# Performance work log

Measured on AMD Instinct MI355X. Metric: run time of the kernel, lower is better.

The kernel has to match this reference:

```python
import jax, jax.numpy as jnp
import numpy as np

IN_SIZE = 1024
HIDDEN = 50
OUT_DIM = 8
BATCH = 16384
BN_EPS = 1e-5


def _gf(h, W1, b1, W2, b2):
    # graph_fusion: Linear -> LeakyReLU(0.2) -> Linear -> Tanh
    t = h @ W1 + b1
    t = jnp.where(t > 0, t, 0.2 * t)
    return jnp.tanh(t @ W2 + b2)


def _lrelu(z):
    return jnp.where(z > 0, z, 0.01 * z)  # F.leaky_relu default slope


def _dot(p, q):
    return jnp.sum(p * q, axis=-1)  # batched [B,1,D]@[B,D,1] -> [B]


def setup_inputs() -> dict:
    key = jax.random.key(0)
    ks = jax.random.split(key, 16)
    d, h, o = IN_SIZE, HIDDEN, OUT_DIM
    s = lambda n: 1.0 / np.sqrt(n)
    return {
        "x": jax.random.normal(ks[0], (BATCH, 3, d), jnp.float32),
        "att_W": jax.random.normal(ks[1], (d, 1), jnp.float32) * s(d),
        "att_b": jnp.zeros((1,), jnp.float32),
        "gf_W1": jax.random.normal(ks[2], (2 * d, 64), jnp.float32) * s(2 * d),
        "gf_b1": jnp.zeros((64,), jnp.float32),
        "gf_W2": jax.random.normal(ks[3], (64, d), jnp.float32) * s(64),
        "gf_b2": jnp.zeros((d,), jnp.float32),
        "bn_gamma": jnp.ones((3 * d,), jnp.float32),
        "bn_beta": jnp.zeros((3 * d,), jnp.float32),
        "l1_W": jax.random.normal(ks[4], (3 * d, h), jnp.float32) * s(3 * d),
        "l1_b": jnp.zeros((h,), jnp.float32),
        "l2_W": jax.random.normal(ks[5], (h, h), jnp.float32) * s(h),
        "l2_b": jnp.zeros((h,), jnp.float32),
        "l3_W": jax.random.normal(ks[6], (h, o), jnp.float32) * s(h),
        "l3_b": jnp.zeros((o,), jnp.float32),
    }


def _forward(x, att_W, att_b, gf_W1, gf_b1, gf_W2, gf_b2,
             bn_gamma, bn_beta, l1_W, l1_b, l2_W, l2_b, l3_W, l3_b):
    a1, v1, l1_ = x[:, 0, :], x[:, 1, :], x[:, 2, :]
    gf = lambda p, q: _gf(jnp.concatenate([p, q], axis=1), gf_W1, gf_b1, gf_W2, gf_b2)

    # unimodal attention weights, softmax over the 3 modalities
    att = jnp.tanh(x @ att_W + att_b)[..., 0]          # [B,3]
    w_uni = jax.nn.softmax(att, axis=1)                # [B,3]
    sa, sv, sl = w_uni[:, 0], w_uni[:, 1], w_uni[:, 2]
    unimodal = (sa[:, None] * a1 + sv[:, None] * v1 + sl[:, None] * l1_) / 3.0

    a = jax.nn.softmax(a1, axis=1)
    v = jax.nn.softmax(v1, axis=1)
    l = jax.nn.softmax(l1_, axis=1)
    sav = (sa + sv) / (_dot(a, v) + 0.5)
    sal = (sa + sl) / (_dot(a, l) + 0.5)
    svl = (sl + sv) / (_dot(v, l) + 0.5)
    w_bi = jax.nn.softmax(jnp.stack([sav, sal, svl], axis=1), axis=1)  # [B,3]

    a_v = _lrelu(w_bi[:, 0:1] * gf(a1, v1))
    a_l = _lrelu(w_bi[:, 1:2] * gf(a1, l1_))
    v_l = _lrelu(w_bi[:, 2:3] * gf(v1, l1_))
    bimodal = (a_v + a_l + v_l) / 3.0

    a_v2 = jax.nn.softmax(a_v, axis=1)
    a_l2 = jax.nn.softmax(a_l, axis=1)
    v_l2 = jax.nn.softmax(v_l, axis=1)
    savvl = (sav + svl) / (_dot(a_v2, v_l2) + 0.5)
    saavl = (sav + sal) / (_dot(a_v2, a_l2) + 0.5)
    savll = (sal + svl) / (_dot(a_l2, v_l2) + 0.5)
    savl = (sav + sl) / (_dot(a_v2, l) + 0.5)
    salv = (sal + sv) / (_dot(a_l2, v) + 0.5)
    svla = (sa + svl) / (_dot(v_l2, a) + 0.5)
    w_tri = jax.nn.softmax(
        jnp.stack([savvl, saavl, savll, savl, salv, svla], axis=1), axis=1)  # [B,6]

    avvl = _lrelu(w_tri[:, 0:1] * gf(a_v, v_l))
    aavl = _lrelu(w_tri[:, 1:2] * gf(a_v, a_l))
    avll = _lrelu(w_tri[:, 2:3] * gf(v_l, a_l))
    avl = _lrelu(w_tri[:, 3:4] * gf(a_v, l1_))
    alv = _lrelu(w_tri[:, 4:5] * gf(a_l, v1))
    vla = _lrelu(w_tri[:, 5:6] * gf(v_l, a1))
    trimodal = (avvl + aavl + avll + avl + alv + vla) / 6.0

    fusion = jnp.concatenate([unimodal, bimodal, trimodal], axis=1)  # [B,3*in]
    # BatchNorm1d in eval mode: running_mean=0, running_var=1
    fusion = fusion * (bn_gamma / jnp.sqrt(1.0 + BN_EPS)) + bn_beta
    y = jnp.tanh(fusion @ l1_W + l1_b)
    y = jnp.tanh(y @ l2_W + l2_b)
    y2 = jax.nn.softmax(y @ l3_W + l3_b, axis=1)
    total_weights = jnp.concatenate([w_uni, w_bi, w_tri], axis=1)  # [B,12]
    return y2, total_weights


def reference(x, att_W, att_b, gf_W1, gf_b1, gf_W2, gf_b2,
              bn_gamma, bn_beta, l1_W, l1_b, l2_W, l2_b, l3_W, l3_b):
    return _forward(x, att_W, att_b, gf_W1, gf_b1, gf_W2, gf_b2,
                    bn_gamma, bn_beta, l1_W, l1_b, l2_W, l2_b, l3_W, l3_b)
```

## Files before the change

kernel.cpp:

```cpp
#include <hip/hip_runtime.h>
#include <math.h>

#define NB 16384
#define DD 1024
#define KF 5120

typedef unsigned short u16;
typedef unsigned int u32;
typedef __attribute__((ext_vector_type(8))) short bf16x8;
typedef __attribute__((ext_vector_type(4))) float f32x4;

__device__ __forceinline__ float bf2f(u16 u){
  return __uint_as_float(((unsigned)u) << 16);
}
__device__ __forceinline__ u16 f2bf(float f){
  unsigned u = __float_as_uint(f);
  return (u16)((u + 0x7fffu + ((u >> 16) & 1u)) >> 16);
}
__device__ __forceinline__ u16 f2bf_tr(float f){
  return (u16)(__float_as_uint(f) >> 16);
}
__device__ __forceinline__ u32 pack2bf(float a, float b){
  return (u32)f2bf(a) | ((u32)f2bf(b) << 16);
}
__device__ __forceinline__ float fast_tanh(float x){
  float e = __expf(2.0f * x);
  return 1.0f - 2.0f * __builtin_amdgcn_rcpf(e + 1.0f);
}
__device__ __forceinline__ float wredsum(float x){
  #pragma unroll
  for(int o = 32; o >= 1; o >>= 1) x += __shfl_xor(x, o);
  return x;
}
__device__ __forceinline__ float wredmax(float x){
  #pragma unroll
  for(int o = 32; o >= 1; o >>= 1) x = fmaxf(x, __shfl_xor(x, o));
  return x;
}
__device__ __forceinline__ void gll16(const void* g, void* l){
  __builtin_amdgcn_global_load_lds(
      (const __attribute__((address_space(1))) u32*)g,
      (__attribute__((address_space(3))) u32*)l, 16, 0, 0);
}

__global__ __launch_bounds__(256) void k1_stats(
    const float* __restrict__ x, const float* __restrict__ attW,
    const float* __restrict__ attb, float* __restrict__ stats,
    u16* __restrict__ Fcat, u16* __restrict__ xb, float* __restrict__ tw)
{
  int wave = threadIdx.x >> 6, lane = threadIdx.x & 63;
  int r = blockIdx.x * 4 + wave;
  const float2* xr  = (const float2*)(x + (size_t)r * 3 * DD);
  const float2* aw2 = (const float2*)attW;
  float2 a[8], v[8], l[8];
  float dA=0.f,dV=0.f,dL=0.f, mA=-1e30f,mV=-1e30f,mL=-1e30f;
  #pragma unroll
  for(int i = 0; i < 8; i++){
    int k2 = lane + i*64;
    a[i] = xr[k2]; v[i] = xr[512+k2]; l[i] = xr[1024+k2];
    float2 w = aw2[k2];
    dA = fmaf(a[i].x, w.x, fmaf(a[i].y, w.y, dA));
    dV = fmaf(v[i].x, w.x, fmaf(v[i].y, w.y, dV));
    dL = fmaf(l[i].x, w.x, fmaf(l[i].y, w.y, dL));
    mA = fmaxf(mA, fmaxf(a[i].x, a[i].y));
    mV = fmaxf(mV, fmaxf(v[i].x, v[i].y));
    mL = fmaxf(mL, fmaxf(l[i].x, l[i].y));
  }
  dA = wredsum(dA); dV = wredsum(dV); dL = wredsum(dL);
  mA = wredmax(mA); mV = wredmax(mV); mL = wredmax(mL);

  u32* xbw = (u32*)(xb + (size_t)3*r*DD);
  #pragma unroll
  for(int i = 0; i < 8; i++){
    int k2 = lane + i*64;
    xbw[k2]      = pack2bf(a[i].x, a[i].y);
    xbw[512+k2]  = pack2bf(v[i].x, v[i].y);
    xbw[1024+k2] = pack2bf(l[i].x, l[i].y);
  }

  float Sa=0.f,Sv=0.f,Sl=0.f,Eav=0.f,Eal=0.f,Evl=0.f;
  #pragma unroll
  for(int i = 0; i < 8; i++){
    float eax = __expf(a[i].x-mA), eay = __expf(a[i].y-mA);
    float evx = __expf(v[i].x-mV), evy = __expf(v[i].y-mV);
    float elx = __expf(l[i].x-mL), ely = __expf(l[i].y-mL);
    Sa += eax+eay; Sv += evx+evy; Sl += elx+ely;
    Eav += eax*evx + eay*evy; Eal += eax*elx + eay*ely; Evl += evx*elx + evy*ely;
  }
  Sa = wredsum(Sa); Sv = wredsum(Sv); Sl = wredsum(Sl);
  Eav = wredsum(Eav); Eal = wredsum(Eal); Evl = wredsum(Evl);

  float ab = attb[0];
  float ta = fast_tanh(dA + ab), tv = fast_tanh(dV + ab), tl = fast_tanh(dL + ab);
  float mm = fmaxf(ta, fmaxf(tv, tl));
  float e0 = __expf(ta-mm), e1 = __expf(tv-mm), e2 = __expf(tl-mm);
  float ss = e0 + e1 + e2;
  float sa = e0/ss, sv = e1/ss, sl = e2/ss;
  float dav = Eav/(Sa*Sv), dal = Eal/(Sa*Sl), dvl = Evl/(Sv*Sl);
  float sav = (sa+sv)/(dav+0.5f);
  float sal = (sa+sl)/(dal+0.5f);
  float svl = (sv+sl)/(dvl+0.5f);
  float m2 = fmaxf(sav, fmaxf(sal, svl));
  float f0 = __expf(sav-m2), f1 = __expf(sal-m2), f2 = __expf(svl-m2);
  float s2 = f0 + f1 + f2;
  float wb0 = f0/s2, wb1 = f1/s2, wb2 = f2/s2;

  if(lane == 0){
    float* st = stats + (size_t)r*24;
    st[0]=sa; st[1]=sv; st[2]=sl;
    st[3]=wb0; st[4]=wb1; st[5]=wb2;
    st[6]=sav; st[7]=sal; st[8]=svl;
    st[9]=mA; st[10]=Sa; st[11]=mV; st[12]=Sv; st[13]=mL; st[14]=Sl;
    float* twr = tw + (size_t)r*12;
    twr[0]=sa; twr[1]=sv; twr[2]=sl; twr[3]=wb0; twr[4]=wb1; twr[5]=wb2;
  }
  u32* uniw = (u32*)(Fcat + (size_t)r*KF);
  #pragma unroll
  for(int i = 0; i < 8; i++){
    int k2 = lane + i*64;
    float ux = (sa*a[i].x + sv*v[i].x + sl*l[i].x) * (1.0f/3.0f);
    float uy = (sa*a[i].y + sv*v[i].y + sl*l[i].y) * (1.0f/3.0f);
    uniw[k2] = pack2bf(ux, uy);
  }
}

__global__ __launch_bounds__(256) void kprew_b1(
    const float* __restrict__ W1, u16* __restrict__ Wb1)
{
  int idx = blockIdx.x * 256 + threadIdx.x;
  int n = idx >> 10, k = idx & 1023;
  float v = (n < 64) ? W1[(size_t)k*64 + n] : W1[(size_t)(1024+k)*64 + (n-64)];
  Wb1[idx] = f2bf(v);
}

__global__ __launch_bounds__(256) void kprew_w2t(
    const float* __restrict__ W2, u16* __restrict__ W2T)
{
  int idx = blockIdx.x * 256 + threadIdx.x;
  int c = idx >> 6, k = idx & 63;
  W2T[idx] = f2bf(W2[(size_t)k*DD + c]);
}

template<int FCAT>
__global__ __launch_bounds__(256) void kg1v3(
    const u16* __restrict__ src, const u16* __restrict__ Wb1,
    float* __restrict__ UV)
{
  __shared__ u16 Asm[2][64*64];
  int tid = threadIdx.x;
  int wv = tid >> 6, lane = tid & 63;
  int fr = lane & 15, kg = lane >> 4;
  int mb = blockIdx.x * 64;

  int r8 = lane >> 3, p = lane & 7;
  int sp = p ^ r8;
  int m0 = mb + (2*wv)*8 + r8;
  int m1 = mb + (2*wv+1)*8 + r8;
  size_t b0, b1;
  if(FCAT){
    int R0 = m0/3, R1 = m1/3;
    b0 = (size_t)R0*KF + (size_t)(1 + (m0 - 3*R0))*1024;
    b1 = (size_t)R1*KF + (size_t)(1 + (m1 - 3*R1))*1024;
  } else {
    b0 = (size_t)m0*1024;
    b1 = (size_t)m1*1024;
  }
  const u16* gsrc0 = src + b0 + sp*8;
  const u16* gsrc1 = src + b1 + sp*8;

  f32x4 acc[4][2];
  #pragma unroll
  for(int rf = 0; rf < 4; rf++)
    #pragma unroll
    for(int nf = 0; nf < 2; nf++) acc[rf][nf] = (f32x4){0.f,0.f,0.f,0.f};

  gll16(gsrc0, &Asm[0][(2*wv)*512]);
  gll16(gsrc1, &Asm[0][(2*wv+1)*512]);
  __syncthreads();

  int buf = 0;
  for(int ci = 0; ci < 16; ci++){
    int k0 = ci*64;
    if(ci < 15){
      gll16(gsrc0 + k0 + 64, &Asm[buf^1][(2*wv)*512]);
      gll16(gsrc1 + k0 + 64, &Asm[buf^1][(2*wv+1)*512]);
    }
    #pragma unroll
    for(int ks = 0; ks < 2; ks++){
      bf16x8 a[4];
      #pragma unroll
      for(int rf = 0; rf < 4; rf++){
        int row = rf*16 + fr;
        int slot = (ks*4 + kg) ^ (row & 7);
        a[rf] = *(const bf16x8*)&Asm[buf][row*64 + slot*8];
      }
      #pragma unroll
      for(int nf = 0; nf < 2; nf++){
        int col = wv*32 + nf*16 + fr;
        bf16x8 b = *(const bf16x8*)&Wb1[(size_t)col*1024 + k0 + ks*32 + kg*8];
        #pragma unroll
        for(int rf = 0; rf < 4; rf++)
          acc[rf][nf] = __builtin_amdgcn_mfma_f32_16x16x32_bf16(a[rf], b, acc[rf][nf], 0, 0, 0);
      }
    }
    __syncthreads();
    buf ^= 1;
  }

  #pragma unroll
  for(int rf = 0; rf < 4; rf++)
    #pragma unroll
    for(int nf = 0; nf < 2; nf++)
      #pragma unroll
      for(int q = 0; q < 4; q++)
        UV[(size_t)(mb + rf*16 + kg*4 + q)*128 + wv*32 + nf*16 + fr] = acc[rf][nf][q];
}

template<int P, int SUM>
__global__ __launch_bounds__(256) void kL2v4(
    const float* __restrict__ UVA, const float* __restrict__ UVB,
    const u16* __restrict__ W2T, const float* __restrict__ b1,
    const float* __restrict__ b2, const float* __restrict__ stats,
    u16* __restrict__ Fcat)
{
  const int NP = SUM ? 1 : P;
  __shared__ u16 Tsm[P][16][64];
  __shared__ u16 Osm[NP][16][264];
  __shared__ float stw[16][8];
  int tid = threadIdx.x;
  int wv = tid >> 6, lane = tid & 63;
  int fr = lane & 15, kg = lane >> 4;
  int Rb = blockIdx.x * 16;
  int cb = blockIdx.y * 256 + wv * 64;

  const int NG = P*16*8;
  for(int i = tid; i < NG; i += 256){
    int g = i & 7, r = (i >> 3) & 15, p = i >> 7;
    int R = Rb + r;
    int up, vp; const float* VBb;
    if(P == 3){
      up = (p == 2) ? 1 : 0;
      vp = (p == 0) ? 1 : 2;
      VBb = UVA;
    } else {
      up = (0x210200 >> (p*4)) & 15;
      vp = (0x012112 >> (p*4)) & 15;
      VBb = (p < 3) ? UVA : UVB;
    }
    const float* Up = UVA + (size_t)(3*R + up)*128 + g*8;
    const float* Vp = VBb + (size_t)(3*R + vp)*128 + 64 + g*8;
    float4 u0 = *(const float4*)Up, u1 = *(const float4*)(Up+4);
    float4 v0 = *(const float4*)Vp, v1 = *(const float4*)(Vp+4);
    float4 bb0 = *(const float4*)(b1 + g*8), bb1 = *(const float4*)(b1 + g*8 + 4);
    float t[8] = {u0.x+v0.x+bb0.x, u0.y+v0.y+bb0.y, u0.z+v0.z+bb0.z, u0.w+v0.w+bb0.w,
                  u1.x+v1.x+bb1.x, u1.y+v1.y+bb1.y, u1.z+v1.z+bb1.z, u1.w+v1.w+bb1.w};
    bf16x8 o;
    #pragma unroll
    for(int j = 0; j < 8; j++){
      float tv = t[j] > 0.f ? t[j] : 0.2f*t[j];
      o[j] = (short)f2bf_tr(tv);
    }
    *(bf16x8*)&Tsm[p][r][(g ^ (r & 7))*8] = o;
  }
  if(tid < 16*P){
    int r = tid / P, p = tid - r*P;
    stw[r][p] = stats[(size_t)(Rb + r)*24 + (SUM ? 15 : 3) + p];
  }
  __syncthreads();

  f32x4 acc[P][4];
  #pragma unroll
  for(int p = 0; p < P; p++)
    #pragma unroll
    for(int cf = 0; cf < 4; cf++) acc[p][cf] = (f32x4){0.f,0.f,0.f,0.f};

  #pragma unroll
  for(int ks = 0; ks < 2; ks++){
    bf16x8 a[P];
    #pragma unroll
    for(int p = 0; p < P; p++)
      a[p] = *(const bf16x8*)&Tsm[p][fr][(((ks<<2)+kg) ^ (fr & 7))*8];
    #pragma unroll
    for(int cf = 0; cf < 4; cf++){
      bf16x8 b = *(const bf16x8*)&W2T[(size_t)(cb + cf*16 + fr)*64 + ks*32 + kg*8];
      #pragma unroll
      for(int p = 0; p < P; p++)
        acc[p][cf] = __builtin_amdgcn_mfma_f32_16x16x32_bf16(a[p], b, acc[p][cf], 0, 0, 0);
    }
  }

  #pragma unroll
  for(int q = 0; q < 4; q++){
    int row = kg*4 + q;
    #pragma unroll
    for(int cf = 0; cf < 4; cf++){
      int cloc = wv*64 + cf*16 + fr;
      float b2c = b2[blockIdx.y*256 + cloc];
      if(SUM){
        float s = 0.f;
        #pragma unroll
        for(int p = 0; p < P; p++){
          float g = stw[row][p] * fast_tanh(acc[p][cf][q] + b2c);
          s += g > 0.f ? g : 0.01f*g;
        }
        Osm[0][row][cloc] = f2bf(s * (1.0f/6.0f));
      } else {
        #pragma unroll
        for(int p = 0; p < P; p++){
          float g = stw[row][p] * fast_tanh(acc[p][cf][q] + b2c);
          float val = g > 0.f ? g : 0.01f*g;
          Osm[p][row][cloc] = f2bf(val);
        }
      }
    }
  }
  __syncthreads();
  {
    int orow = tid >> 4, oc16 = (tid & 15) * 16;
    #pragma unroll
    for(int p = 0; p < NP; p++){
      bf16x8 o0 = *(const bf16x8*)&Osm[p][orow][oc16];
      bf16x8 o1 = *(const bf16x8*)&Osm[p][orow][oc16 + 8];
      size_t off = (size_t)(Rb + orow)*KF + (SUM ? 4096 : (size_t)(1+p)*1024)
                 + blockIdx.y*256 + oc16;
      *(bf16x8*)&Fcat[off]     = o0;
      *(bf16x8*)&Fcat[off + 8] = o1;
    }
  }
}

__global__ __launch_bounds__(256) void k3s_stats2(
    const u16* __restrict__ Fcat, const u16* __restrict__ xb,
    float* __restrict__ stats, float* __restrict__ tw)
{
  int wave = threadIdx.x >> 6, lane = threadIdx.x & 63;
  int r = blockIdx.x * 4 + wave;
  const u32* pv = (const u32*)(Fcat + (size_t)r*KF + 1024);
  const u32* xv = (const u32*)(xb + (size_t)3*r*DD);
  float2 av[8], al[8], vl[8];
  float mav=-1e30f, mal=-1e30f, mvl=-1e30f;
  #pragma unroll
  for(int i = 0; i < 8; i++){
    int k2 = lane + i*64;
    u32 wa = pv[k2], wb = pv[512+k2], wc = pv[1024+k2];
    av[i] = make_float2(bf2f((u16)wa), bf2f((u16)(wa>>16)));
    al[i] = make_float2(bf2f((u16)wb), bf2f((u16)(wb>>16)));
    vl[i] = make_float2(bf2f((u16)wc), bf2f((u16)(wc>>16)));
    mav = fmaxf(mav, fmaxf(av[i].x, av[i].y));
    mal = fmaxf(mal, fmaxf(al[i].x, al[i].y));
    mvl = fmaxf(mvl, fmaxf(vl[i].x, vl[i].y));
  }
  mav = wredmax(mav); mal = wredmax(mal); mvl = wredmax(mvl);

  float* st = stats + (size_t)r*24;
  float sa=st[0], sv=st[1], sl=st[2];
  float sav=st[6], sal=st[7], svl=st[8];
  float mA=st[9], Sa=st[10], mV=st[11], Sv=st[12], mL=st[13], Sl=st[14];

  float Savv=0.f,Sall=0.f,Svll=0.f,E1=0.f,E2=0.f,E3=0.f,E4=0.f,E5=0.f,E6=0.f;
  #pragma unroll
  for(int i = 0; i < 8; i++){
    int k2 = lane + i*64;
    u32 xa = xv[k2], xvv = xv[512+k2], xl = xv[1024+k2];
    float a1x = bf2f((u16)xa),  a1y = bf2f((u16)(xa>>16));
    float v1x = bf2f((u16)xvv), v1y = bf2f((u16)(xvv>>16));
    float l1x = bf2f((u16)xl),  l1y = bf2f((u16)(xl>>16));
    float eavx = __expf(av[i].x-mav), eavy = __expf(av[i].y-mav);
    float ealx = __expf(al[i].x-mal), ealy = __expf(al[i].y-mal);
    float evlx = __expf(vl[i].x-mvl), evly = __expf(vl[i].y-mvl);
    Savv += eavx+eavy; Sall += ealx+ealy; Svll += evlx+evly;
    float eax = __expf(a1x-mA), eay = __expf(a1y-mA);
    float evx = __expf(v1x-mV), evy = __expf(v1y-mV);
    float elx = __expf(l1x-mL), ely = __expf(l1y-mL);
    E1 += eavx*evlx + eavy*evly; E2 += eavx*ealx + eavy*ealy; E3 += ealx*evlx + ealy*evly;
    E4 += eavx*elx + eavy*ely;   E5 += ealx*evx + ealy*evy;   E6 += evlx*eax + evly*eay;
  }
  Savv = wredsum(Savv); Sall = wredsum(Sall); Svll = wredsum(Svll);
  E1 = wredsum(E1); E2 = wredsum(E2); E3 = wredsum(E3);
  E4 = wredsum(E4); E5 = wredsum(E5); E6 = wredsum(E6);

  float d1 = E1/(Savv*Svll), d2 = E2/(Savv*Sall), d3 = E3/(Sall*Svll);
  float d4 = E4/(Savv*Sl),   d5 = E5/(Sall*Sv),   d6 = E6/(Svll*Sa);
  float t0 = (sav+svl)/(d1+0.5f);
  float t1 = (sav+sal)/(d2+0.5f);
  float t2 = (sal+svl)/(d3+0.5f);
  float t3 = (sav+sl)/(d4+0.5f);
  float t4 = (sal+sv)/(d5+0.5f);
  float t5 = (sa+svl)/(d6+0.5f);
  float mx = fmaxf(fmaxf(fmaxf(t0,t1),fmaxf(t2,t3)),fmaxf(t4,t5));
  float g0=__expf(t0-mx),g1=__expf(t1-mx),g2=__expf(t2-mx);
  float g3=__expf(t3-mx),g4=__expf(t4-mx),g5=__expf(t5-mx);
  float gs = g0+g1+g2+g3+g4+g5;
  if(lane == 0){
    float wt[6] = {g0/gs,g1/gs,g2/gs,g3/gs,g4/gs,g5/gs};
    float* twr = tw + (size_t)r*12;
    #pragma unroll
    for(int p = 0; p < 6; p++){ st[15+p] = wt[p]; twr[6+p] = wt[p]; }
  }
}

__global__ __launch_bounds__(256) void k6_prew(
    const float* __restrict__ gamma, const float* __restrict__ l1W,
    u16* __restrict__ WpT)
{
  int kk = blockIdx.x * 256 + threadIdx.x;
  int j  = blockIdx.y;
  const float gsc = 1.0f / sqrtf(1.0f + 1e-5f);
  int korig; float sc;
  if(kk < 1024){ korig = kk; sc = 1.f; }
  else if(kk < 4096){ korig = 1024 + ((kk - 1024) & 1023); sc = 1.0f/3.0f; }
  else { korig = 2048 + (kk - 4096); sc = 1.f; }
  float v = (j < 50) ? l1W[(size_t)korig*50 + j] * gamma[korig] * gsc * sc : 0.f;
  WpT[(size_t)j*KF + kk] = f2bf(v);
}

__global__ __launch_bounds__(256) void k6_preb(
    const float* __restrict__ beta, const float* __restrict__ l1W,
    const float* __restrict__ l1b, float* __restrict__ bp)
{
  __shared__ float red[4][64];
  int j = threadIdx.x & 63, seg = threadIdx.x >> 6;
  float s = 0.f;
  if(j < 50){
    for(int k = seg*768; k < seg*768 + 768; k++)
      s = fmaf(beta[k], l1W[(size_t)k*50 + j], s);
  }
  red[seg][j] = s;
  __syncthreads();
  if(seg == 0){
    float t = red[0][j] + red[1][j] + red[2][j] + red[3][j];
    bp[j] = (j < 50) ? (l1b[j] + t) : 0.f;
  }
}

__global__ __launch_bounds__(256) void k6v4(
    const u16* __restrict__ Fcat, const u16* __restrict__ WpT,
    const float* __restrict__ bp,
    const float* __restrict__ l2W, const float* __restrict__ l2b,
    const float* __restrict__ l3W, const float* __restrict__ l3b,
    float* __restrict__ y2out)
{
  __shared__ __align__(16) char smem[37952];
  u16*  Asm = (u16*)smem;
  float* W2s = (float*)(smem + 16384);
  float* W3s = (float*)(smem + 16384 + 12800);
  float* Ys  = (float*)smem;
  float* Ys2 = (float*)(smem + 16384 + 12800 + 1600);

  int tid = threadIdx.x;
  int wv = tid >> 6, lane = tid & 63;
  int fr = lane & 15, kg = lane >> 4;
  int rb = blockIdx.x * 32;

  for(int t = tid; t < 3200; t += 256){
    int c = t & 63;
    W2s[t] = (c < 50) ? l2W[(t >> 6)*50 + c] : 0.f;
  }
  for(int t = tid; t < 400; t += 256) W3s[t] = l3W[t];

  int r8 = lane >> 3, pp = lane & 7;
  int sp = pp ^ r8;
  const u16* gsrc = Fcat + (size_t)(rb + wv*8 + r8)*KF + sp*8;
  const u16* bptr = WpT  + (size_t)(wv*16 + fr)*KF + kg*8;

  f32x4 acc[2];
  acc[0] = (f32x4){0.f,0.f,0.f,0.f};
  acc[1] = (f32x4){0.f,0.f,0.f,0.f};

  gll16(gsrc,      &Asm[wv*1024]);
  gll16(gsrc + 64, &Asm[wv*1024 + 512]);
  __syncthreads();

  int buf = 0;
  for(int ci = 0; ci < 40; ci++){
    int k0 = ci*128;
    if(ci < 39){
      gll16(gsrc + k0 + 128, &Asm[(buf^1)*4096 + wv*1024]);
      gll16(gsrc + k0 + 192, &Asm[(buf^1)*4096 + wv*1024 + 512]);
    }
    #pragma unroll
    for(int kh = 0; kh < 2; kh++){
      #pragma unroll
      for(int ks = 0; ks < 2; ks++){
        bf16x8 b = *(const bf16x8*)(bptr + k0 + kh*64 + ks*32);
        #pragma unroll
        for(int rf = 0; rf < 2; rf++){
          int row = rf*16 + fr;
          int slot = ((ks<<2) + kg) ^ (row & 7);
          bf16x8 a = *(const bf16x8*)&Asm[buf*4096 + (row>>3)*1024 + kh*512
                                          + (row & 7)*64 + slot*8];
          acc[rf] = __builtin_amdgcn_mfma_f32_16x16x32_bf16(a, b, acc[rf], 0, 0, 0);
        }
      }
    }
    __syncthreads();
    buf ^= 1;
  }

  {
    int col = wv*16 + fr;
    float bpc = bp[col];
    #pragma unroll
    for(int rf = 0; rf < 2; rf++)
      #pragma unroll
      for(int q = 0; q < 4; q++){
        int row = rf*16 + kg*4 + q;
        if(col < 50) Ys[row*56 + col] = fast_tanh(acc[rf][q] + bpc);
      }
  }
  __syncthreads();

  {
    int r = tid >> 3, cg = (tid & 7) * 7;
    float a2[7] = {0,0,0,0,0,0,0};
    for(int k = 0; k < 50; k++){
      float yv = Ys[r*56 + k];
      #pragma unroll
      for(int c = 0; c < 7; c++) a2[c] = fmaf(yv, W2s[k*64 + cg + c], a2[c]);
    }
    #pragma unroll
    for(int c = 0; c < 7; c++){
      int cc = cg + c;
      if(cc < 50) Ys2[r*56 + cc] = fast_tanh(a2[c] + l2b[cc]);
    }
  }
  __syncthreads();

  {
    int r = tid >> 3, c = tid & 7;
    float z = l3b[c];
    for(int k = 0; k < 50; k++) z = fmaf(Ys2[r*56 + k], W3s[k*8 + c], z);
    float m = z;
    m = fmaxf(m, __shfl_xor(m, 1));
    m = fmaxf(m, __shfl_xor(m, 2));
    m = fmaxf(m, __shfl_xor(m, 4));
    float e = __expf(z - m);
    float s = e;
    s += __shfl_xor(s, 1); s += __shfl_xor(s, 2); s += __shfl_xor(s, 4);
    y2out[(size_t)(rb + r)*8 + c] = e / s;
  }
}

extern "C" void kernel_launch(void* const* d_in, const int* in_sizes, int n_in,
                              void* d_out, int out_size, void* d_ws, size_t ws_size,
                              hipStream_t stream)
{
  (void)in_sizes; (void)n_in; (void)out_size; (void)ws_size;
  const float* x    = (const float*)d_in[0];
  const float* attW = (const float*)d_in[1];
  const float* attb = (const float*)d_in[2];
  const float* gfW1 = (const float*)d_in[3];
  const float* gfb1 = (const float*)d_in[4];
  const float* gfW2 = (const float*)d_in[5];
  const float* gfb2 = (const float*)d_in[6];
  const float* bng  = (const float*)d_in[7];
  const float* bnb  = (const float*)d_in[8];
  const float* l1W  = (const float*)d_in[9];
  const float* l1b  = (const float*)d_in[10];
  const float* l2W  = (const float*)d_in[11];
  const float* l2b  = (const float*)d_in[12];
  const float* l3W  = (const float*)d_in[13];
  const float* l3b  = (const float*)d_in[14];

  float* out = (float*)d_out;
  float* tw  = out + (size_t)NB*8;

  float* ws    = (float*)d_ws;
  float* stats = ws;
  float* UV1   = stats + (size_t)NB*24;
  float* UV2   = UV1 + (size_t)3*NB*128;
  float* bp    = UV2 + (size_t)3*NB*128;
  u16* WpT     = (u16*)(bp + 64);
  u16* Wb1     = WpT + (size_t)64*KF;
  u16* W2T     = Wb1 + (size_t)128*1024;
  u16* Fcat    = W2T + (size_t)1024*64;
  u16* xb      = Fcat + (size_t)NB*KF;

  k1_stats<<<dim3(NB/4), dim3(256), 0, stream>>>(x, attW, attb, stats, Fcat, xb, tw);
  kprew_b1<<<dim3(512), dim3(256), 0, stream>>>(gfW1, Wb1);
  kprew_w2t<<<dim3(256), dim3(256), 0, stream>>>(gfW2, W2T);
  k6_prew<<<dim3(20, 64), dim3(256), 0, stream>>>(bng, l1W, WpT);
  k6_preb<<<dim3(1), dim3(256), 0, stream>>>(bnb, l1W, l1b, bp);

  kg1v3<0><<<dim3(3*NB/64), dim3(256), 0, stream>>>(xb, Wb1, UV1);
  kL2v4<3,0><<<dim3(NB/16, 4), dim3(256), 0, stream>>>(UV1, UV1, W2T, gfb1, gfb2, stats, Fcat);
  k3s_stats2<<<dim3(NB/4), dim3(256), 0, stream>>>(Fcat, xb, stats, tw);
  kg1v3<1><<<dim3(3*NB/64), dim3(256), 0, stream>>>(Fcat, Wb1, UV2);
  kL2v4<6,1><<<dim3(NB/16, 4), dim3(256), 0, stream>>>(UV2, UV1, W2T, gfb1, gfb2, stats, Fcat);
  k6v4<<<dim3(NB/32), dim3(256), 0, stream>>>(Fcat, WpT, bp, l2W, l2b, l3W, l3b, out);
}
```

Baseline: 406.7 us.

## Fuse fusion-layer partial GEMM into gf epilogues with atomic accumulation

The bimodal and trimodal contributions to the first classifier layer are now computed inside the graph-fusion epilogue kernels. Each block multiplies its output tile by the matching slice of the folded weight and atomically adds the result into a per-row accumulator. The final kernel therefore only streams the unimodal 1024 columns instead of the full 5120-wide concatenation. The trimodal block is no longer written to the concat buffer, and the weight-prep kernels are merged into one launch. The stats2 kernel also drops its max-subtraction pass for the bimodal softmaxes, which relies on those values being bounded, and the change adds atomic traffic plus some bf16 truncation.

```diff
diff --git a/kernel.cpp b/kernel.cpp
--- a/kernel.cpp
+++ b/kernel.cpp
@@ -43,10 +43,57 @@
       (__attribute__((address_space(3))) u32*)l, 16, 0, 0);
 }
 
+__global__ __launch_bounds__(256) void kpre(
+    const float* __restrict__ W1, const float* __restrict__ W2,
+    const float* __restrict__ gamma, const float* __restrict__ beta,
+    const float* __restrict__ l1W, const float* __restrict__ l1b,
+    u16* __restrict__ Wb1, u16* __restrict__ W2T, u16* __restrict__ WpT,
+    float* __restrict__ bp, float* __restrict__ y1g)
+{
+  __shared__ float red[4][64];
+  int b = blockIdx.x, tid = threadIdx.x;
+  if(b < 512){
+    int idx = b*256 + tid;
+    int n = idx >> 10, k = idx & 1023;
+    float v = (n < 64) ? W1[(size_t)k*64 + n] : W1[(size_t)(1024+k)*64 + (n-64)];
+    Wb1[idx] = f2bf(v);
+  } else if(b < 768){
+    int idx = (b-512)*256 + tid;
+    int c = idx >> 6, k = idx & 63;
+    W2T[idx] = f2bf(W2[(size_t)k*DD + c]);
+  } else if(b < 768 + 1280){
+    int idx = (b-768)*256 + tid;
+    int j = idx / KF, kk = idx - j*KF;
+    const float gsc = 1.0f / sqrtf(1.0f + 1e-5f);
+    int korig; float sc;
+    if(kk < 1024){ korig = kk; sc = 1.f; }
+    else if(kk < 4096){ korig = 1024 + ((kk - 1024) & 1023); sc = 1.0f/3.0f; }
+    else { korig = 2048 + (kk - 4096); sc = 1.f; }
+    float v = (j < 50) ? l1W[(size_t)korig*50 + j] * gamma[korig] * gsc * sc : 0.f;
+    WpT[(size_t)j*KF + kk] = f2bf(v);
+  } else if(b < 768 + 1280 + 1024){
+    int idx = (b - 2048)*256 + tid;
+    ((float4*)y1g)[idx] = make_float4(0.f,0.f,0.f,0.f);
+  } else {
+    int j = tid & 63, seg = tid >> 6;
+    float s = 0.f;
+    if(j < 50){
+      for(int k = seg*768; k < seg*768 + 768; k++)
+        s = fmaf(beta[k], l1W[(size_t)k*50 + j], s);
+    }
+    red[seg][j] = s;
+    __syncthreads();
+    if(seg == 0){
+      float t = red[0][j] + red[1][j] + red[2][j] + red[3][j];
+      bp[j] = (j < 50) ? (l1b[j] + t) : 0.f;
+    }
+  }
+}
+
 __global__ __launch_bounds__(256) void k1_stats(
     const float* __restrict__ x, const float* __restrict__ attW,
     const float* __restrict__ attb, float* __restrict__ stats,
-    u16* __restrict__ Fcat, u16* __restrict__ xb, float* __restrict__ tw)
+    u16* __restrict__ uniB, u16* __restrict__ xb, float* __restrict__ tw)
 {
   int wave = threadIdx.x >> 6, lane = threadIdx.x & 63;
   int r = blockIdx.x * 4 + wave;
@@ -114,7 +161,7 @@
     float* twr = tw + (size_t)r*12;
     twr[0]=sa; twr[1]=sv; twr[2]=sl; twr[3]=wb0; twr[4]=wb1; twr[5]=wb2;
   }
-  u32* uniw = (u32*)(Fcat + (size_t)r*KF);
+  u32* uniw = (u32*)(uniB + (size_t)r*DD);
   #pragma unroll
   for(int i = 0; i < 8; i++){
     int k2 = lane + i*64;
@@ -122,23 +169,6 @@
     float uy = (sa*a[i].y + sv*v[i].y + sl*l[i].y) * (1.0f/3.0f);
     uniw[k2] = pack2bf(ux, uy);
   }
-}
-
-__global__ __launch_bounds__(256) void kprew_b1(
-    const float* __restrict__ W1, u16* __restrict__ Wb1)
-{
-  int idx = blockIdx.x * 256 + threadIdx.x;
-  int n = idx >> 10, k = idx & 1023;
-  float v = (n < 64) ? W1[(size_t)k*64 + n] : W1[(size_t)(1024+k)*64 + (n-64)];
-  Wb1[idx] = f2bf(v);
-}
-
-__global__ __launch_bounds__(256) void kprew_w2t(
-    const float* __restrict__ W2, u16* __restrict__ W2T)
-{
-  int idx = blockIdx.x * 256 + threadIdx.x;
-  int c = idx >> 6, k = idx & 63;
-  W2T[idx] = f2bf(W2[(size_t)k*DD + c]);
 }
 
 template<int FCAT>
@@ -217,21 +247,21 @@
 }
 
 template<int P, int SUM>
-__global__ __launch_bounds__(256) void kL2v4(
+__global__ __launch_bounds__(256) void kL2v5(
     const float* __restrict__ UVA, const float* __restrict__ UVB,
-    const u16* __restrict__ W2T, const float* __restrict__ b1,
-    const float* __restrict__ b2, const float* __restrict__ stats,
-    u16* __restrict__ Fcat)
-{
-  const int NP = SUM ? 1 : P;
+    const u16* __restrict__ W2T, const u16* __restrict__ WpT,
+    const float* __restrict__ b1, const float* __restrict__ b2,
+    const float* __restrict__ stats, u16* __restrict__ Fcat,
+    float* __restrict__ y1g)
+{
+  const int NO = SUM ? 1 : 4;
   __shared__ u16 Tsm[P][16][64];
-  __shared__ u16 Osm[NP][16][264];
+  __shared__ u16 Osm[NO][16][264];
   __shared__ float stw[16][8];
   int tid = threadIdx.x;
   int wv = tid >> 6, lane = tid & 63;
   int fr = lane & 15, kg = lane >> 4;
   int Rb = blockIdx.x * 16;
-  int cb = blockIdx.y * 256 + wv * 64;
 
   const int NG = P*16*8;
   for(int i = tid; i < NG; i += 256){
@@ -282,7 +312,8 @@
       a[p] = *(const bf16x8*)&Tsm[p][fr][(((ks<<2)+kg) ^ (fr & 7))*8];
     #pragma unroll
     for(int cf = 0; cf < 4; cf++){
-      bf16x8 b = *(const bf16x8*)&W2T[(size_t)(cb + cf*16 + fr)*64 + ks*32 + kg*8];
+      bf16x8 b = *(const bf16x8*)&W2T[(size_t)(blockIdx.y*256 + wv*64 + cf*16 + fr)*64
+                                      + ks*32 + kg*8];
       #pragma unroll
       for(int p = 0; p < P; p++)
         acc[p][cf] = __builtin_amdgcn_mfma_f32_16x16x32_bf16(a[p], b, acc[p][cf], 0, 0, 0);
@@ -303,33 +334,53 @@
           float g = stw[row][p] * fast_tanh(acc[p][cf][q] + b2c);
           s += g > 0.f ? g : 0.01f*g;
         }
-        Osm[0][row][cloc] = f2bf(s * (1.0f/6.0f));
+        Osm[0][row][cloc] = f2bf_tr(s * (1.0f/6.0f));
       } else {
+        float sm = 0.f;
         #pragma unroll
         for(int p = 0; p < P; p++){
           float g = stw[row][p] * fast_tanh(acc[p][cf][q] + b2c);
           float val = g > 0.f ? g : 0.01f*g;
           Osm[p][row][cloc] = f2bf(val);
+          sm += val;
         }
+        Osm[3][row][cloc] = f2bf_tr(sm);
       }
     }
   }
   __syncthreads();
-  {
+
+  if(!SUM){
     int orow = tid >> 4, oc16 = (tid & 15) * 16;
     #pragma unroll
-    for(int p = 0; p < NP; p++){
+    for(int p = 0; p < 3; p++){
       bf16x8 o0 = *(const bf16x8*)&Osm[p][orow][oc16];
       bf16x8 o1 = *(const bf16x8*)&Osm[p][orow][oc16 + 8];
-      size_t off = (size_t)(Rb + orow)*KF + (SUM ? 4096 : (size_t)(1+p)*1024)
-                 + blockIdx.y*256 + oc16;
+      size_t off = (size_t)(Rb + orow)*KF + (size_t)(1+p)*1024 + blockIdx.y*256 + oc16;
       *(bf16x8*)&Fcat[off]     = o0;
       *(bf16x8*)&Fcat[off + 8] = o1;
     }
   }
-}
-
-__global__ __launch_bounds__(256) void k3s_stats2(
+
+  {
+    size_t kbase = (SUM ? 4096 : 1024) + (size_t)blockIdx.y*256;
+    const u16* bptr = WpT + (size_t)(wv*16 + fr)*KF + kbase + kg*8;
+    f32x4 accy = (f32x4){0.f,0.f,0.f,0.f};
+    #pragma unroll
+    for(int kq = 0; kq < 4; kq++)
+      #pragma unroll
+      for(int ks = 0; ks < 2; ks++){
+        bf16x8 a = *(const bf16x8*)&Osm[NO-1][fr][kq*64 + ks*32 + kg*8];
+        bf16x8 b = *(const bf16x8*)(bptr + kq*64 + ks*32);
+        accy = __builtin_amdgcn_mfma_f32_16x16x32_bf16(a, b, accy, 0, 0, 0);
+      }
+    #pragma unroll
+    for(int q = 0; q < 4; q++)
+      atomicAdd(&y1g[(size_t)(Rb + kg*4 + q)*64 + wv*16 + fr], accy[q]);
+  }
+}
+
+__global__ __launch_bounds__(256) void k3s_v2(
     const u16* __restrict__ Fcat, const u16* __restrict__ xb,
     float* __restrict__ stats, float* __restrict__ tw)
 {
@@ -337,20 +388,6 @@
   int r = blockIdx.x * 4 + wave;
   const u32* pv = (const u32*)(Fcat + (size_t)r*KF + 1024);
   const u32* xv = (const u32*)(xb + (size_t)3*r*DD);
-  float2 av[8], al[8], vl[8];
-  float mav=-1e30f, mal=-1e30f, mvl=-1e30f;
-  #pragma unroll
-  for(int i = 0; i < 8; i++){
-    int k2 = lane + i*64;
-    u32 wa = pv[k2], wb = pv[512+k2], wc = pv[1024+k2];
-    av[i] = make_float2(bf2f((u16)wa), bf2f((u16)(wa>>16)));
-    al[i] = make_float2(bf2f((u16)wb), bf2f((u16)(wb>>16)));
-    vl[i] = make_float2(bf2f((u16)wc), bf2f((u16)(wc>>16)));
-    mav = fmaxf(mav, fmaxf(av[i].x, av[i].y));
-    mal = fmaxf(mal, fmaxf(al[i].x, al[i].y));
-    mvl = fmaxf(mvl, fmaxf(vl[i].x, vl[i].y));
-  }
-  mav = wredmax(mav); mal = wredmax(mal); mvl = wredmax(mvl);
 
   float* st = stats + (size_t)r*24;
   float sa=st[0], sv=st[1], sl=st[2];
@@ -361,17 +398,15 @@
   #pragma unroll
   for(int i = 0; i < 8; i++){
     int k2 = lane + i*64;
+    u32 wa = pv[k2], wb = pv[512+k2], wc = pv[1024+k2];
     u32 xa = xv[k2], xvv = xv[512+k2], xl = xv[1024+k2];
-    float a1x = bf2f((u16)xa),  a1y = bf2f((u16)(xa>>16));
-    float v1x = bf2f((u16)xvv), v1y = bf2f((u16)(xvv>>16));
-    float l1x = bf2f((u16)xl),  l1y = bf2f((u16)(xl>>16));
-    float eavx = __expf(av[i].x-mav), eavy = __expf(av[i].y-mav);
-    float ealx = __expf(al[i].x-mal), ealy = __expf(al[i].y-mal);
-    float evlx = __expf(vl[i].x-mvl), evly = __expf(vl[i].y-mvl);
+    float eavx = __expf(bf2f((u16)wa)),      eavy = __expf(bf2f((u16)(wa>>16)));
+    float ealx = __expf(bf2f((u16)wb)),      ealy = __expf(bf2f((u16)(wb>>16)));
+    float evlx = __expf(bf2f((u16)wc)),      evly = __expf(bf2f((u16)(wc>>16)));
+    float eax  = __expf(bf2f((u16)xa)-mA),   eay  = __expf(bf2f((u16)(xa>>16))-mA);
+    float evx  = __expf(bf2f((u16)xvv)-mV),  evy  = __expf(bf2f((u16)(xvv>>16))-mV);
+    float elx  = __expf(bf2f((u16)xl)-mL),   ely  = __expf(bf2f((u16)(xl>>16))-mL);
     Savv += eavx+eavy; Sall += ealx+ealy; Svll += evlx+evly;
-    float eax = __expf(a1x-mA), eay = __expf(a1y-mA);
-    float evx = __expf(v1x-mV), evy = __expf(v1y-mV);
-    float elx = __expf(l1x-mL), ely = __expf(l1y-mL);
     E1 += eavx*evlx + eavy*evly; E2 += eavx*ealx + eavy*ealy; E3 += ealx*evlx + ealy*evly;
     E4 += eavx*elx + eavy*ely;   E5 += ealx*evx + ealy*evy;   E6 += evlx*eax + evly*eay;
   }
@@ -399,43 +434,9 @@
   }
 }
 
-__global__ __launch_bounds__(256) void k6_prew(
-    const float* __restrict__ gamma, const float* __restrict__ l1W,
-    u16* __restrict__ WpT)
-{
-  int kk = blockIdx.x * 256 + threadIdx.x;
-  int j  = blockIdx.y;
-  const float gsc = 1.0f / sqrtf(1.0f + 1e-5f);
-  int korig; float sc;
-  if(kk < 1024){ korig = kk; sc = 1.f; }
-  else if(kk < 4096){ korig = 1024 + ((kk - 1024) & 1023); sc = 1.0f/3.0f; }
-  else { korig = 2048 + (kk - 4096); sc = 1.f; }
-  float v = (j < 50) ? l1W[(size_t)korig*50 + j] * gamma[korig] * gsc * sc : 0.f;
-  WpT[(size_t)j*KF + kk] = f2bf(v);
-}
-
-__global__ __launch_bounds__(256) void k6_preb(
-    const float* __restrict__ beta, const float* __restrict__ l1W,
-    const float* __restrict__ l1b, float* __restrict__ bp)
-{
-  __shared__ float red[4][64];
-  int j = threadIdx.x & 63, seg = threadIdx.x >> 6;
-  float s = 0.f;
-  if(j < 50){
-    for(int k = seg*768; k < seg*768 + 768; k++)
-      s = fmaf(beta[k], l1W[(size_t)k*50 + j], s);
-  }
-  red[seg][j] = s;
-  __syncthreads();
-  if(seg == 0){
-    float t = red[0][j] + red[1][j] + red[2][j] + red[3][j];
-    bp[j] = (j < 50) ? (l1b[j] + t) : 0.f;
-  }
-}
-
-__global__ __launch_bounds__(256) void k6v4(
-    const u16* __restrict__ Fcat, const u16* __restrict__ WpT,
-    const float* __restrict__ bp,
+__global__ __launch_bounds__(256) void k6v5(
+    const u16* __restrict__ uniB, const u16* __restrict__ WpT,
+    const float* __restrict__ y1g, const float* __restrict__ bp,
     const float* __restrict__ l2W, const float* __restrict__ l2b,
     const float* __restrict__ l3W, const float* __restrict__ l3b,
     float* __restrict__ y2out)
@@ -460,7 +461,7 @@
 
   int r8 = lane >> 3, pp = lane & 7;
   int sp = pp ^ r8;
-  const u16* gsrc = Fcat + (size_t)(rb + wv*8 + r8)*KF + sp*8;
+  const u16* gsrc = uniB + (size_t)(rb + wv*8 + r8)*DD + sp*8;
   const u16* bptr = WpT  + (size_t)(wv*16 + fr)*KF + kg*8;
 
   f32x4 acc[2];
@@ -472,9 +473,9 @@
   __syncthreads();
 
   int buf = 0;
-  for(int ci = 0; ci < 40; ci++){
+  for(int ci = 0; ci < 8; ci++){
     int k0 = ci*128;
-    if(ci < 39){
+    if(ci < 7){
       gll16(gsrc + k0 + 128, &Asm[(buf^1)*4096 + wv*1024]);
       gll16(gsrc + k0 + 192, &Asm[(buf^1)*4096 + wv*1024 + 512]);
     }
@@ -505,7 +506,10 @@
       #pragma unroll
       for(int q = 0; q < 4; q++){
         int row = rf*16 + kg*4 + q;
-        if(col < 50) Ys[row*56 + col] = fast_tanh(acc[rf][q] + bpc);
+        if(col < 50){
+          float z = acc[rf][q] + y1g[(size_t)(rb + row)*64 + col] + bpc;
+          Ys[row*56 + col] = fast_tanh(z);
+        }
       }
   }
   __syncthreads();
@@ -570,22 +574,25 @@
   float* UV1   = stats + (size_t)NB*24;
   float* UV2   = UV1 + (size_t)3*NB*128;
   float* bp    = UV2 + (size_t)3*NB*128;
-  u16* WpT     = (u16*)(bp + 64);
+  float* y1g   = bp + 64;
+  u16* WpT     = (u16*)(y1g + (size_t)NB*64);
   u16* Wb1     = WpT + (size_t)64*KF;
   u16* W2T     = Wb1 + (size_t)128*1024;
   u16* Fcat    = W2T + (size_t)1024*64;
   u16* xb      = Fcat + (size_t)NB*KF;
-
-  k1_stats<<<dim3(NB/4), dim3(256), 0, stream>>>(x, attW, attb, stats, Fcat, xb, tw);
-  kprew_b1<<<dim3(512), dim3(256), 0, stream>>>(gfW1, Wb1);
-  kprew_w2t<<<dim3(256), dim3(256), 0, stream>>>(gfW2, W2T);
-  k6_prew<<<dim3(20, 64), dim3(256), 0, stream>>>(bng, l1W, WpT);
-  k6_preb<<<dim3(1), dim3(256), 0, stream>>>(bnb, l1W, l1b, bp);
+  u16* uniB    = xb + (size_t)3*NB*DD;
+
+  kpre<<<dim3(768 + 1280 + 1024 + 1), dim3(256), 0, stream>>>(
+      gfW1, gfW2, bng, bnb, l1W, l1b, Wb1, W2T, WpT, bp, y1g);
+  k1_stats<<<dim3(NB/4), dim3(256), 0, stream>>>(x, attW, attb, stats, uniB, xb, tw);
 
   kg1v3<0><<<dim3(3*NB/64), dim3(256), 0, stream>>>(xb, Wb1, UV1);
-  kL2v4<3,0><<<dim3(NB/16, 4), dim3(256), 0, stream>>>(UV1, UV1, W2T, gfb1, gfb2, stats, Fcat);
-  k3s_stats2<<<dim3(NB/4), dim3(256), 0, stream>>>(Fcat, xb, stats, tw);
+  kL2v5<3,0><<<dim3(NB/16, 4), dim3(256), 0, stream>>>(UV1, UV1, W2T, WpT,
+                                                       gfb1, gfb2, stats, Fcat, y1g);
+  k3s_v2<<<dim3(NB/4), dim3(256), 0, stream>>>(Fcat, xb, stats, tw);
   kg1v3<1><<<dim3(3*NB/64), dim3(256), 0, stream>>>(Fcat, Wb1, UV2);
-  kL2v4<6,1><<<dim3(NB/16, 4), dim3(256), 0, stream>>>(UV2, UV1, W2T, gfb1, gfb2, stats, Fcat);
-  k6v4<<<dim3(NB/32), dim3(256), 0, stream>>>(Fcat, WpT, bp, l2W, l2b, l3W, l3b, out);
-}
+  kL2v5<6,1><<<dim3(NB/16, 4), dim3(256), 0, stream>>>(UV2, UV1, W2T, WpT,
+                                                       gfb1, gfb2, stats, Fcat, y1g);
+  k6v5<<<dim3(NB/32), dim3(256), 0, stream>>>(uniB, WpT, y1g, bp,
+                                              l2W, l2b, l3W, l3b, out);
+}
```

Result: faster. 392.6 us (-3.5%).
